# Optimization experiments

Measured on AMD Instinct MI355X. Metric: run time of the kernel, lower is better.

## Reference

```python
import jax, jax.numpy as jnp
import numpy as np

D_MODEL = 2048
N_HEADS = 16
D_HEAD = D_MODEL // N_HEADS
FF = 4 * D_MODEL
ROPE_BASE = 10000.0


def setup_inputs() -> dict:
    key = jax.random.key(0)
    ks = jax.random.split(key, 12)
    s = 0.02
    B, S = 2, 2048
    return {
        "x": jax.random.normal(ks[0], (B, S, D_MODEL), dtype=jnp.float32),
        # torch Linear layout: [out_features, in_features]
        "w_qkv": jax.random.normal(ks[1], (3 * D_MODEL, D_MODEL), dtype=jnp.float32) * s,
        "w_proj": jax.random.normal(ks[2], (D_MODEL, D_MODEL), dtype=jnp.float32) * s,
        "b_proj": jnp.zeros((D_MODEL,), dtype=jnp.float32),
        "w_ff1": jax.random.normal(ks[3], (FF, D_MODEL), dtype=jnp.float32) * s,
        "b_ff1": jnp.zeros((FF,), dtype=jnp.float32),
        "w_ff2": jax.random.normal(ks[4], (D_MODEL, FF), dtype=jnp.float32) * s,
        "b_ff2": jnp.zeros((D_MODEL,), dtype=jnp.float32),
        "g1": jnp.ones((D_MODEL,), dtype=jnp.float32),
        "beta1": jnp.zeros((D_MODEL,), dtype=jnp.float32),
        "g2": jnp.ones((D_MODEL,), dtype=jnp.float32),
        "beta2": jnp.zeros((D_MODEL,), dtype=jnp.float32),
    }


def _layer_norm(x, g, b, eps=1e-5):
    mu = jnp.mean(x, axis=-1, keepdims=True)
    var = jnp.var(x, axis=-1, keepdims=True)
    return (x - mu) * jax.lax.rsqrt(var + eps) * g + b


def _rope_cos_sin(seq_len, dtype):
    inv_freq = 1.0 / (ROPE_BASE ** (jnp.arange(0, D_HEAD, 2, dtype=jnp.float32) / D_HEAD))
    t = jnp.arange(seq_len, dtype=jnp.float32)
    freqs = jnp.einsum("i,j->ij", t, inv_freq)  # [S, D_HEAD//2]
    emb = jnp.concatenate([freqs, freqs], axis=-1)  # [S, D_HEAD]
    return jnp.cos(emb).astype(dtype), jnp.sin(emb).astype(dtype)


def _rotate_half(x):
    x1, x2 = x[..., : D_HEAD // 2], x[..., D_HEAD // 2 :]
    return jnp.concatenate([-x2, x1], axis=-1)


def reference(x, w_qkv, w_proj, b_proj, w_ff1, b_ff1, w_ff2, b_ff2, g1, beta1, g2, beta2):
    B, S, _ = x.shape
    # --- attention block ---
    h = _layer_norm(x, g1, beta1)
    qkv = h @ w_qkv.T  # [B,S,3D]
    xq, xk, xv = jnp.split(qkv, 3, axis=-1)
    xq = xq.reshape(B, S, N_HEADS, D_HEAD)
    xk = xk.reshape(B, S, N_HEADS, D_HEAD)
    xv = xv.reshape(B, S, N_HEADS, D_HEAD)
    cos, sin = _rope_cos_sin(S, x.dtype)
    cos = cos[None, :, None, :]  # [1,S,1,Dh]
    sin = sin[None, :, None, :]
    xq = xq * cos + _rotate_half(xq) * sin
    xk = xk * cos + _rotate_half(xk) * sin
    # SDPA, causal
    scale = 1.0 / jnp.sqrt(jnp.asarray(D_HEAD, dtype=x.dtype))
    scores = jnp.einsum("bqhd,bkhd->bhqk", xq, xk) * scale  # [B,H,S,S]
    causal = jnp.tril(jnp.ones((S, S), dtype=bool))
    scores = jnp.where(causal[None, None], scores, jnp.finfo(x.dtype).min)
    att = jax.nn.softmax(scores, axis=-1)
    out = jnp.einsum("bhqk,bkhd->bqhd", att, xv).reshape(B, S, D_MODEL)
    att_out = out @ w_proj.T + b_proj
    x = x + att_out
    # --- feed-forward block (exact GELU, matching nn.GELU default) ---
    h = _layer_norm(x, g2, beta2)
    ff = jax.nn.gelu(h @ w_ff1.T + b_ff1, approximate=False) @ w_ff2.T + b_ff2
    return x + ff
```

## Files before the change

kernel.cpp:

```cpp
#include <hip/hip_runtime.h>
#include <hip/hip_bf16.h>
#include <cmath>

#define D_MODEL 2048
#define N_HEADS 16
#define D_HEAD  128
#define FFDIM   8192
#define BATCH   2
#define SEQ     2048
#define TOKENS  (BATCH * SEQ)

using bf16 = __hip_bfloat16;
typedef __bf16 v8bf __attribute__((ext_vector_type(8)));
typedef float  v4f  __attribute__((ext_vector_type(4)));

__global__ __launch_bounds__(256) void cast_kernel(const float* __restrict__ in,
                                                   bf16* __restrict__ out, int n4) {
    int i = blockIdx.x * 256 + threadIdx.x;
    if (i < n4) {
        float4 f = ((const float4*)in)[i];
        int o = i * 4;
        out[o + 0] = __float2bfloat16(f.x);
        out[o + 1] = __float2bfloat16(f.y);
        out[o + 2] = __float2bfloat16(f.z);
        out[o + 3] = __float2bfloat16(f.w);
    }
}

__global__ __launch_bounds__(256) void ln_kernel(const float* __restrict__ x,
                                                 const float* __restrict__ g,
                                                 const float* __restrict__ b,
                                                 bf16* __restrict__ out) {
    int row = blockIdx.x;
    int t = threadIdx.x;
    const float* xr = x + (size_t)row * D_MODEL;
    float v[8];
    float s = 0.f, s2 = 0.f;
#pragma unroll
    for (int i = 0; i < 8; i++) {
        float val = xr[t + 256 * i];
        v[i] = val;
        s += val;
        s2 += val * val;
    }
#pragma unroll
    for (int off = 32; off > 0; off >>= 1) {
        s  += __shfl_down(s, off, 64);
        s2 += __shfl_down(s2, off, 64);
    }
    __shared__ float ws1[4], ws2[4];
    int wv = t >> 6;
    if ((t & 63) == 0) { ws1[wv] = s; ws2[wv] = s2; }
    __syncthreads();
    float fs  = ws1[0] + ws1[1] + ws1[2] + ws1[3];
    float fs2 = ws2[0] + ws2[1] + ws2[2] + ws2[3];
    float mean = fs * (1.0f / D_MODEL);
    float var  = fs2 * (1.0f / D_MODEL) - mean * mean;
    float rstd = rsqrtf(var + 1e-5f);
    bf16* orow = out + (size_t)row * D_MODEL;
#pragma unroll
    for (int i = 0; i < 8; i++) {
        int c = t + 256 * i;
        orow[c] = __float2bfloat16((v[i] - mean) * rstd * g[c] + b[c]);
    }
}

__global__ __launch_bounds__(256) void rope_kernel(bf16* __restrict__ qkv) {
    int unit = blockIdx.x * 4 + (threadIdx.x >> 6);
    int j = threadIdx.x & 63;
    int h = unit & (N_HEADS - 1);
    int tok = unit >> 4;
    int pos = tok & (SEQ - 1);
    float invf = powf(10000.0f, -(float)j / 64.0f);
    float ang = (float)pos * invf;
    float c = cosf(ang), s = sinf(ang);
    const float sc = 0.08838834764831845f;
    size_t base = (size_t)tok * (3 * D_MODEL) + h * D_HEAD;
    float q1 = __bfloat162float(qkv[base + j]), q2 = __bfloat162float(qkv[base + j + 64]);
    qkv[base + j]      = __float2bfloat16((q1 * c - q2 * s) * sc);
    qkv[base + j + 64] = __float2bfloat16((q2 * c + q1 * s) * sc);
    size_t kb = base + D_MODEL;
    float k1 = __bfloat162float(qkv[kb + j]), k2 = __bfloat162float(qkv[kb + j + 64]);
    qkv[kb + j]      = __float2bfloat16(k1 * c - k2 * s);
    qkv[kb + j + 64] = __float2bfloat16(k2 * c + k1 * s);
}

__global__ __launch_bounds__(256) void vt_kernel(const bf16* __restrict__ qkv,
                                                 bf16* __restrict__ vt) {
    __shared__ float tile[32][65];
    int bh = blockIdx.x;
    int k0 = blockIdx.y * 64;
    int d0 = blockIdx.z * 32;
    int b = bh >> 4, h = bh & 15;
    int t = threadIdx.x;
    const bf16* src = qkv + ((size_t)b * SEQ + k0) * (3 * D_MODEL) + 2 * D_MODEL + h * D_HEAD + d0;
#pragma unroll
    for (int i = 0; i < 8; i++) {
        int e = t + 256 * i;
        int kr = e >> 5, dc = e & 31;
        tile[dc][kr] = __bfloat162float(src[(size_t)kr * (3 * D_MODEL) + dc]);
    }
    __syncthreads();
    bf16* dst = vt + ((size_t)bh * D_HEAD + d0) * SEQ + k0;
#pragma unroll
    for (int i = 0; i < 8; i++) {
        int e = t + 256 * i;
        int dr = e >> 6, kc = e & 63;
        dst[(size_t)dr * SEQ + kc] = __float2bfloat16(tile[dr][kc]);
    }
}

#define KS_STRIDE 136
#define VT_STRIDE 72
#define PS_STRIDE 72

__global__ __launch_bounds__(256) void flash_attn(const bf16* __restrict__ qkv,
                                                  const bf16* __restrict__ vt,
                                                  bf16* __restrict__ att) {
    __shared__ __align__(16) bf16 Ks[64 * KS_STRIDE];
    __shared__ __align__(16) bf16 Vts[D_HEAD * VT_STRIDE];
    __shared__ __align__(16) bf16 Ps[4 * 16 * PS_STRIDE];

    int bh = blockIdx.x;
    int qt = (int)gridDim.y - 1 - (int)blockIdx.y;
    int b = bh >> 4, h = bh & 15;
    int t = threadIdx.x, wave = t >> 6, lane = t & 63;
    int lr = lane & 15, lq = lane >> 4;

    const bf16* qp = qkv + ((size_t)b * SEQ + qt * 64 + wave * 16 + lr) * (3 * D_MODEL) + h * D_HEAD;
    v8bf aq[4];
#pragma unroll
    for (int c = 0; c < 4; c++)
        aq[c] = *(const v8bf*)(qp + c * 32 + lq * 8);

    float m_r[4], l_r[4];
    v4f O[8] = {};
#pragma unroll
    for (int r = 0; r < 4; r++) { m_r[r] = -1e30f; l_r[r] = 0.f; }

    int n_tiles = qt + 1;
    for (int kt = 0; kt < n_tiles; kt++) {
        int kv0 = kt * 64;
        __syncthreads();
        {
            const bf16* kbase = qkv + ((size_t)b * SEQ + kv0) * (3 * D_MODEL) + D_MODEL + h * D_HEAD;
#pragma unroll
            for (int i = 0; i < 4; i++) {
                int e = t + 256 * i;
                int kr = e >> 4, c8 = (e & 15) * 8;
                *(uint4*)&Ks[kr * KS_STRIDE + c8] = *(const uint4*)(kbase + (size_t)kr * (3 * D_MODEL) + c8);
            }
            const bf16* vbase = vt + (size_t)bh * D_HEAD * SEQ + kv0;
#pragma unroll
            for (int i = 0; i < 4; i++) {
                int e8 = t + 256 * i;
                int dr = e8 >> 3, k8 = (e8 & 7) * 8;
                *(uint4*)&Vts[dr * VT_STRIDE + k8] = *(const uint4*)(vbase + (size_t)dr * SEQ + k8);
            }
        }
        __syncthreads();

        v4f sc[4];
#pragma unroll
        for (int nt = 0; nt < 4; nt++) {
            v4f a = {};
#pragma unroll
            for (int c = 0; c < 4; c++) {
                v8bf bk = *(const v8bf*)&Ks[(nt * 16 + lr) * KS_STRIDE + c * 32 + lq * 8];
                a = __builtin_amdgcn_mfma_f32_16x16x32_bf16(aq[c], bk, a, 0, 0, 0);
            }
            sc[nt] = a;
        }
        if (kt == n_tiles - 1) {
#pragma unroll
            for (int nt = 0; nt < 4; nt++)
#pragma unroll
                for (int r = 0; r < 4; r++) {
                    int cl = nt * 16 + lr, rl = wave * 16 + lq * 4 + r;
                    if (cl > rl) sc[nt][r] = -1e30f;
                }
        }
        float mt[4];
#pragma unroll
        for (int r = 0; r < 4; r++) {
            float v = fmaxf(fmaxf(sc[0][r], sc[1][r]), fmaxf(sc[2][r], sc[3][r]));
#pragma unroll
            for (int mk = 8; mk >= 1; mk >>= 1) v = fmaxf(v, __shfl_xor(v, mk, 64));
            mt[r] = v;
        }
        float alpha[4];
#pragma unroll
        for (int r = 0; r < 4; r++) {
            float mn = fmaxf(m_r[r], mt[r]);
            alpha[r] = __expf(m_r[r] - mn);
            m_r[r] = mn;
        }
        bf16* pw = &Ps[wave * 16 * PS_STRIDE];
        float rs[4] = {0.f, 0.f, 0.f, 0.f};
#pragma unroll
        for (int nt = 0; nt < 4; nt++)
#pragma unroll
            for (int r = 0; r < 4; r++) {
                float p = __expf(sc[nt][r] - m_r[r]);
                rs[r] += p;
                pw[(lq * 4 + r) * PS_STRIDE + nt * 16 + lr] = __float2bfloat16(p);
            }
#pragma unroll
        for (int r = 0; r < 4; r++) {
            float v = rs[r];
#pragma unroll
            for (int mk = 8; mk >= 1; mk >>= 1) v += __shfl_xor(v, mk, 64);
            l_r[r] = l_r[r] * alpha[r] + v;
        }
#pragma unroll
        for (int jt = 0; jt < 8; jt++)
#pragma unroll
            for (int r = 0; r < 4; r++) O[jt][r] *= alpha[r];

        asm volatile("s_waitcnt lgkmcnt(0)" ::: "memory");

        v8bf ap[2];
#pragma unroll
        for (int c = 0; c < 2; c++)
            ap[c] = *(const v8bf*)&pw[lr * PS_STRIDE + c * 32 + lq * 8];
#pragma unroll
        for (int jt = 0; jt < 8; jt++) {
#pragma unroll
            for (int c = 0; c < 2; c++) {
                v8bf bv = *(const v8bf*)&Vts[(jt * 16 + lr) * VT_STRIDE + c * 32 + lq * 8];
                O[jt] = __builtin_amdgcn_mfma_f32_16x16x32_bf16(ap[c], bv, O[jt], 0, 0, 0);
            }
        }
    }

    float inv[4];
#pragma unroll
    for (int r = 0; r < 4; r++) inv[r] = 1.0f / l_r[r];
#pragma unroll
    for (int jt = 0; jt < 8; jt++)
#pragma unroll
        for (int r = 0; r < 4; r++) {
            size_t idx = ((size_t)b * SEQ + qt * 64 + wave * 16 + lq * 4 + r) * D_MODEL + h * D_HEAD + jt * 16 + lr;
            att[idx] = __float2bfloat16(O[jt][r] * inv[r]);
        }
}

#define BM 128
#define BN 128
#define BK 32

template <int EPI>
__global__ __launch_bounds__(256) void gemm_bt(const bf16* __restrict__ A,
                                               const bf16* __restrict__ W,
                                               const float* __restrict__ bias,
                                               const float* __restrict__ res,
                                               float* __restrict__ outF,
                                               bf16* __restrict__ outB,
                                               int M, int N, int K) {
    __shared__ __align__(16) bf16 As[BM * BK];
    __shared__ __align__(16) bf16 Bs[BN * BK];
    int t = threadIdx.x;
    int wave = t >> 6, lane = t & 63;
    int wm = (wave >> 1) * 64;
    int wn = (wave & 1) * 64;
    int lr = lane & 15;
    int lq = lane >> 4;

    int nbx = gridDim.x;
    int bid = (int)blockIdx.y * nbx + (int)blockIdx.x;
    int per = (nbx * (int)gridDim.y) >> 3;
    int lbid = (bid & 7) * per + (bid >> 3);
    const int GM = 8;
    int pw = GM * nbx;
    int panel = lbid / pw;
    int rem = lbid - panel * pw;
    int bm = panel * GM + (rem & (GM - 1));
    int bn = rem >> 3;
    int row0 = bm * BM;
    int col0 = bn * BN;

    int lr4 = lane >> 2;
    int lc8 = (lane & 3) * 8;

    v4f acc[4][4] = {};

    for (int k0 = 0; k0 < K; k0 += BK) {
#pragma unroll
        for (int u = 0; u < 2; u++) {
            int c = wave * 2 + u;
            const bf16* ga = A + (size_t)(row0 + c * 16 + lr4) * K + k0 + lc8;
            __builtin_amdgcn_global_load_lds(
                (const __attribute__((address_space(1))) void*)ga,
                (__attribute__((address_space(3))) void*)&As[c * 512], 16, 0, 0);
            const bf16* gb = W + (size_t)(col0 + c * 16 + lr4) * K + k0 + lc8;
            __builtin_amdgcn_global_load_lds(
                (const __attribute__((address_space(1))) void*)gb,
                (__attribute__((address_space(3))) void*)&Bs[c * 512], 16, 0, 0);
        }
        __syncthreads();
        v8bf af[4], bfr[4];
#pragma unroll
        for (int i = 0; i < 4; i++) {
            af[i]  = *(const v8bf*)(&As[(wm + i * 16 + lr) * BK + lq * 8]);
            bfr[i] = *(const v8bf*)(&Bs[(wn + i * 16 + lr) * BK + lq * 8]);
        }
#pragma unroll
        for (int i = 0; i < 4; i++)
#pragma unroll
            for (int j = 0; j < 4; j++)
                acc[i][j] = __builtin_amdgcn_mfma_f32_16x16x32_bf16(af[i], bfr[j], acc[i][j], 0, 0, 0);
        __syncthreads();
    }

#pragma unroll
    for (int i = 0; i < 4; i++) {
#pragma unroll
        for (int j = 0; j < 4; j++) {
#pragma unroll
            for (int r = 0; r < 4; r++) {
                int grow = row0 + wm + i * 16 + lq * 4 + r;
                int gcol = col0 + wn + j * 16 + lr;
                float c = acc[i][j][r];
                size_t idx = (size_t)grow * N + gcol;
                if (EPI == 0) {
                    outF[idx] = c;
                } else if (EPI == 1) {
                    outF[idx] = c + bias[gcol] + res[idx];
                } else if (EPI == 2) {
                    c += bias[gcol];
                    float gel = 0.5f * c * (1.0f + erff(c * 0.7071067811865475f));
                    outB[idx] = __float2bfloat16(gel);
                } else {
                    outB[idx] = __float2bfloat16(c);
                }
            }
        }
    }
}

extern "C" void kernel_launch(void* const* d_in, const int* in_sizes, int n_in,
                              void* d_out, int out_size, void* d_ws, size_t ws_size,
                              hipStream_t stream) {
    const float* x      = (const float*)d_in[0];
    const float* w_qkv  = (const float*)d_in[1];
    const float* w_proj = (const float*)d_in[2];
    const float* b_proj = (const float*)d_in[3];
    const float* w_ff1  = (const float*)d_in[4];
    const float* b_ff1  = (const float*)d_in[5];
    const float* w_ff2  = (const float*)d_in[6];
    const float* b_ff2  = (const float*)d_in[7];
    const float* g1     = (const float*)d_in[8];
    const float* be1    = (const float*)d_in[9];
    const float* g2     = (const float*)d_in[10];
    const float* be2    = (const float*)d_in[11];
    float* out = (float*)d_out;

    char* ws = (char*)d_ws;
    size_t off = 0;
    auto alloc = [&](size_t bytes) {
        void* p = ws + off;
        off += (bytes + 255) & ~(size_t)255;
        return p;
    };
    bf16*  wqkv_b  = (bf16*)alloc((size_t)3 * D_MODEL * D_MODEL * sizeof(bf16));
    bf16*  wproj_b = (bf16*)alloc((size_t)D_MODEL * D_MODEL * sizeof(bf16));
    bf16*  wff1_b  = (bf16*)alloc((size_t)FFDIM * D_MODEL * sizeof(bf16));
    bf16*  wff2_b  = (bf16*)alloc((size_t)D_MODEL * FFDIM * sizeof(bf16));
    bf16*  qkv_b   = (bf16*)alloc((size_t)TOKENS * FFDIM * sizeof(bf16));
    bf16*  ff1_b   = qkv_b;
    bf16*  act_b   = (bf16*)alloc((size_t)TOKENS * D_MODEL * sizeof(bf16));
    float* x2_f    = (float*)alloc((size_t)TOKENS * D_MODEL * sizeof(float));
    bf16*  vt_g    = (bf16*)x2_f;

    cast_kernel<<<(3 * D_MODEL * D_MODEL / 4 + 255) / 256, 256, 0, stream>>>(w_qkv, wqkv_b, 3 * D_MODEL * D_MODEL / 4);
    cast_kernel<<<(D_MODEL * D_MODEL / 4 + 255) / 256, 256, 0, stream>>>(w_proj, wproj_b, D_MODEL * D_MODEL / 4);
    cast_kernel<<<(FFDIM * D_MODEL / 4 + 255) / 256, 256, 0, stream>>>(w_ff1, wff1_b, FFDIM * D_MODEL / 4);
    cast_kernel<<<(D_MODEL * FFDIM / 4 + 255) / 256, 256, 0, stream>>>(w_ff2, wff2_b, D_MODEL * FFDIM / 4);

    ln_kernel<<<TOKENS, 256, 0, stream>>>(x, g1, be1, act_b);

    gemm_bt<3><<<dim3(3 * D_MODEL / BN, TOKENS / BM), 256, 0, stream>>>(
        act_b, wqkv_b, nullptr, nullptr, nullptr, qkv_b, TOKENS, 3 * D_MODEL, D_MODEL);

    rope_kernel<<<TOKENS * N_HEADS / 4, 256, 0, stream>>>(qkv_b);

    vt_kernel<<<dim3(BATCH * N_HEADS, SEQ / 64, D_HEAD / 32), 256, 0, stream>>>(qkv_b, vt_g);

    flash_attn<<<dim3(BATCH * N_HEADS, SEQ / 64), 256, 0, stream>>>(qkv_b, vt_g, act_b);

    gemm_bt<1><<<dim3(D_MODEL / BN, TOKENS / BM), 256, 0, stream>>>(
        act_b, wproj_b, b_proj, x, x2_f, nullptr, TOKENS, D_MODEL, D_MODEL);

    ln_kernel<<<TOKENS, 256, 0, stream>>>(x2_f, g2, be2, act_b);

    gemm_bt<2><<<dim3(FFDIM / BN, TOKENS / BM), 256, 0, stream>>>(
        act_b, wff1_b, b_ff1, nullptr, nullptr, ff1_b, TOKENS, FFDIM, D_MODEL);

    gemm_bt<1><<<dim3(D_MODEL / BN, TOKENS / BM), 256, 0, stream>>>(
        ff1_b, wff2_b, b_ff2, x2_f, out, nullptr, TOKENS, D_MODEL, FFDIM);

    (void)in_sizes; (void)n_in; (void)out_size; (void)ws_size;
}
```

Before: 1.042 ms.

## Double GEMM K-tile to 64 with XOR-swizzled LDS layout, merge weight casts

The GEMM's K tile grows from 32 to 64, so each loop iteration issues twice as many MFMAs per pair of barriers. The direct global-to-LDS loads now use an XOR swizzle on the 8-element column blocks to avoid LDS bank conflicts on the wider rows. The four per-weight cast kernels are also merged into a single launch. The doubled LDS tile uses more shared memory per block, which can lower occupancy.

Result: faster. 922.0 us (-11.5%).

```diff
diff --git a/kernel.cpp b/kernel.cpp
--- a/kernel.cpp
+++ b/kernel.cpp
@@ -14,17 +14,31 @@
 typedef __bf16 v8bf __attribute__((ext_vector_type(8)));
 typedef float  v4f  __attribute__((ext_vector_type(4)));
 
-__global__ __launch_bounds__(256) void cast_kernel(const float* __restrict__ in,
-                                                   bf16* __restrict__ out, int n4) {
+#define N0 (3 * D_MODEL * D_MODEL / 4)
+#define N1 (D_MODEL * D_MODEL / 4)
+#define N2 (FFDIM * D_MODEL / 4)
+#define N3 (D_MODEL * FFDIM / 4)
+
+__global__ __launch_bounds__(256) void cast4_kernel(const float* __restrict__ w0,
+                                                    const float* __restrict__ w1,
+                                                    const float* __restrict__ w2,
+                                                    const float* __restrict__ w3,
+                                                    bf16* __restrict__ o0,
+                                                    bf16* __restrict__ o1,
+                                                    bf16* __restrict__ o2,
+                                                    bf16* __restrict__ o3) {
     int i = blockIdx.x * 256 + threadIdx.x;
-    if (i < n4) {
-        float4 f = ((const float4*)in)[i];
-        int o = i * 4;
-        out[o + 0] = __float2bfloat16(f.x);
-        out[o + 1] = __float2bfloat16(f.y);
-        out[o + 2] = __float2bfloat16(f.z);
-        out[o + 3] = __float2bfloat16(f.w);
-    }
+    const float* src; bf16* dst; int j;
+    if (i < N0)                { src = w0; dst = o0; j = i; }
+    else if (i < N0 + N1)      { src = w1; dst = o1; j = i - N0; }
+    else if (i < N0 + N1 + N2) { src = w2; dst = o2; j = i - N0 - N1; }
+    else                       { src = w3; dst = o3; j = i - N0 - N1 - N2; }
+    float4 f = ((const float4*)src)[j];
+    int o = j * 4;
+    dst[o + 0] = __float2bfloat16(f.x);
+    dst[o + 1] = __float2bfloat16(f.y);
+    dst[o + 2] = __float2bfloat16(f.z);
+    dst[o + 3] = __float2bfloat16(f.w);
 }
 
 __global__ __launch_bounds__(256) void ln_kernel(const float* __restrict__ x,
@@ -247,7 +261,7 @@
 
 #define BM 128
 #define BN 128
-#define BK 32
+#define BK 64
 
 template <int EPI>
 __global__ __launch_bounds__(256) void gemm_bt(const bf16* __restrict__ A,
@@ -279,36 +293,42 @@
     int row0 = bm * BM;
     int col0 = bn * BN;
 
-    int lr4 = lane >> 2;
-    int lc8 = (lane & 3) * 8;
+    int srow = lane >> 3;
+    int sblk = lane & 7;
+    int scol = ((sblk ^ srow) * 8);
 
     v4f acc[4][4] = {};
 
     for (int k0 = 0; k0 < K; k0 += BK) {
 #pragma unroll
-        for (int u = 0; u < 2; u++) {
-            int c = wave * 2 + u;
-            const bf16* ga = A + (size_t)(row0 + c * 16 + lr4) * K + k0 + lc8;
+        for (int u = 0; u < 4; u++) {
+            int c = wave * 4 + u;
+            const bf16* ga = A + (size_t)(row0 + c * 8 + srow) * K + k0 + scol;
             __builtin_amdgcn_global_load_lds(
                 (const __attribute__((address_space(1))) void*)ga,
                 (__attribute__((address_space(3))) void*)&As[c * 512], 16, 0, 0);
-            const bf16* gb = W + (size_t)(col0 + c * 16 + lr4) * K + k0 + lc8;
+            const bf16* gb = W + (size_t)(col0 + c * 8 + srow) * K + k0 + scol;
             __builtin_amdgcn_global_load_lds(
                 (const __attribute__((address_space(1))) void*)gb,
                 (__attribute__((address_space(3))) void*)&Bs[c * 512], 16, 0, 0);
         }
         __syncthreads();
-        v8bf af[4], bfr[4];
-#pragma unroll
-        for (int i = 0; i < 4; i++) {
-            af[i]  = *(const v8bf*)(&As[(wm + i * 16 + lr) * BK + lq * 8]);
-            bfr[i] = *(const v8bf*)(&Bs[(wn + i * 16 + lr) * BK + lq * 8]);
-        }
-#pragma unroll
-        for (int i = 0; i < 4; i++)
-#pragma unroll
-            for (int j = 0; j < 4; j++)
-                acc[i][j] = __builtin_amdgcn_mfma_f32_16x16x32_bf16(af[i], bfr[j], acc[i][j], 0, 0, 0);
+#pragma unroll
+        for (int half = 0; half < 2; half++) {
+            v8bf af[4], bfr[4];
+            int gblk = half * 4 + lq;
+            int soff = ((gblk ^ (lr & 7)) * 8);
+#pragma unroll
+            for (int i = 0; i < 4; i++) {
+                af[i]  = *(const v8bf*)(&As[(wm + i * 16 + lr) * BK + soff]);
+                bfr[i] = *(const v8bf*)(&Bs[(wn + i * 16 + lr) * BK + soff]);
+            }
+#pragma unroll
+            for (int i = 0; i < 4; i++)
+#pragma unroll
+                for (int j = 0; j < 4; j++)
+                    acc[i][j] = __builtin_amdgcn_mfma_f32_16x16x32_bf16(af[i], bfr[j], acc[i][j], 0, 0, 0);
+        }
         __syncthreads();
     }
 
@@ -372,10 +392,8 @@
     float* x2_f    = (float*)alloc((size_t)TOKENS * D_MODEL * sizeof(float));
     bf16*  vt_g    = (bf16*)x2_f;
 
-    cast_kernel<<<(3 * D_MODEL * D_MODEL / 4 + 255) / 256, 256, 0, stream>>>(w_qkv, wqkv_b, 3 * D_MODEL * D_MODEL / 4);
-    cast_kernel<<<(D_MODEL * D_MODEL / 4 + 255) / 256, 256, 0, stream>>>(w_proj, wproj_b, D_MODEL * D_MODEL / 4);
-    cast_kernel<<<(FFDIM * D_MODEL / 4 + 255) / 256, 256, 0, stream>>>(w_ff1, wff1_b, FFDIM * D_MODEL / 4);
-    cast_kernel<<<(D_MODEL * FFDIM / 4 + 255) / 256, 256, 0, stream>>>(w_ff2, wff2_b, D_MODEL * FFDIM / 4);
+    cast4_kernel<<<N0 + N1 + N2 + N3 >= 0 ? (N0 + N1 + N2 + N3 + 255) / 256 : 0, 256, 0, stream>>>(
+        w_qkv, w_proj, w_ff1, w_ff2, wqkv_b, wproj_b, wff1_b, wff2_b);
 
     ln_kernel<<<TOKENS, 256, 0, stream>>>(x, g1, be1, act_b);
 
```
